# Performance work log

Hardware: AMD Instinct MI355X
Metric: run time of the kernel (lower is better)

The kernel has to match this reference:

```python
import jax, jax.numpy as jnp
import numpy as np

N_POINTS = 8192
N_TOPICS = 64
B = 524288


def setup_inputs() -> dict:
    key = jax.random.key(0)
    k1, k2, k3, k4 = jax.random.split(key, 4)
    pij = jax.random.uniform(k1, (B,), dtype=jnp.float32, minval=1e-6, maxval=1.0)
    i = jax.random.randint(k2, (B,), 0, N_POINTS, dtype=jnp.int64)
    j = jax.random.randint(k3, (B,), 0, N_POINTS, dtype=jnp.int64)
    W = jax.random.normal(k4, (N_POINTS, N_TOPICS), dtype=jnp.float32)  # nn.Embedding weight
    return {"pij": pij, "i": i, "j": j, "W": W}


def reference(pij, i, j, W):
    # pairwise squared distances over ALL points, via the gram trick
    # (avoids materializing the [n, n, d] broadcasted tensor of the torch code)
    sq = jnp.sum(W * W, axis=1)                       # [n]
    d2 = sq[:, None] + sq[None, :] - 2.0 * (W @ W.T)  # [n, n]
    d2 = jnp.maximum(d2, 0.0)                         # numerical floor (exact math is >= 0)
    n = W.shape[0]
    # Cauchy kernel partition: sum_{k,l} 1/(1+d2) minus the n diagonal ones
    part = jnp.sum(1.0 / (1.0 + d2)) - jnp.asarray(n, d2.dtype)
    xi = W[i]                                         # [B, d]
    xj = W[j]                                         # [B, d]
    # FAITHFUL to source: (1 + diff^2).sum(1) adds 1 per dim => n_topics + ||xi-xj||^2
    num = 1.0 / jnp.sum(1.0 + (xi - xj) ** 2, axis=1)  # [B]
    qij = num / part
    loss_kld = pij * (jnp.log(pij) - jnp.log(qij))
    return jnp.sum(loss_kld)
```

## Files before the change

kernel.cpp:

```cpp
#include <hip/hip_runtime.h>
#include <math.h>

#define NPOINTS   8192
#define NDIM      64
#define TILE      128
#define NT2       64
#define NBLK      2080
#define NGRP      512

#define WS_W16   0
#define WS_W8    262144
#define WS_SQ    393216
#define WS_PARTA 401408
#define WS_A1P   403488
#define WS_A3P   407584

typedef __attribute__((ext_vector_type(8))) short bf16x8;
typedef __attribute__((ext_vector_type(4))) float f32x4;
typedef __attribute__((ext_vector_type(2))) float f32x2;

__device__ inline unsigned f2bf_pk(float lo, float hi) {
    unsigned ul = __float_as_uint(lo), uh = __float_as_uint(hi);
    ul += 0x7FFFu + ((ul >> 16) & 1u);
    uh += 0x7FFFu + ((uh >> 16) & 1u);
    return (ul >> 16) | (uh & 0xFFFF0000u);
}
template <bool HI>
__device__ inline f32x2 cvt2(unsigned dw) {
    return __builtin_amdgcn_cvt_pk_f32_fp8((int)dw, HI);
}
__device__ inline void sqacc(f32x2& s, unsigned a, unsigned b) {
    f32x2 dl = cvt2<false>(a) - cvt2<false>(b);
    f32x2 dh = cvt2<true >(a) - cvt2<true >(b);
    s += dl * dl;
    s += dh * dh;
}

__global__ __launch_bounds__(256) void prep_kernel(const float* __restrict__ W,
                                                   float* __restrict__ sq,
                                                   unsigned* __restrict__ W16f,
                                                   unsigned* __restrict__ W8) {
    int g = blockIdx.x;
    int t = threadIdx.x;

    {
        int h = t >> 7, L = (t >> 1) & 63, dp = t & 1;
        int row = g * 16 + (L & 15), quad = L >> 4;
        float4 v = *(const float4*)(W + row * NDIM + h * 32 + quad * 8 + dp * 4);
        uint2 o;
        o.x = f2bf_pk(v.x, v.y);
        o.y = f2bf_pk(v.z, v.w);
        *(uint2*)(W16f + ((g * 2 + h) * 256 + L * 4 + dp * 2)) = o;
    }
    {
        int r = t >> 4, s = t & 15;
        float4 v = *(const float4*)(W + (g * 16 + r) * NDIM + s * 4);
        float p = v.x * v.x + v.y * v.y + v.z * v.z + v.w * v.w;
        p += __shfl_xor(p, 1, 64);
        p += __shfl_xor(p, 2, 64);
        p += __shfl_xor(p, 4, 64);
        p += __shfl_xor(p, 8, 64);
        if (s == 0) sq[g * 16 + r] = p;
    }
    {
        int r = g * 16 + (t >> 4), d = t & 15;
        float4 x = *(const float4*)(W + r * NDIM + d * 4);
        int lo = __builtin_amdgcn_cvt_pk_fp8_f32(x.x, x.y, 0, false);
        int dw = __builtin_amdgcn_cvt_pk_fp8_f32(x.z, x.w, lo, true);
        W8[r * 16 + d] = (unsigned)dw;
    }
}

__global__ __launch_bounds__(256) void pair_kernel(const unsigned* __restrict__ W8,
                                                   const float* __restrict__ pij,
                                                   const int* __restrict__ ii,
                                                   const int* __restrict__ jj,
                                                   int nb,
                                                   float* __restrict__ a1p,
                                                   float* __restrict__ a3p) {
    int t = threadIdx.x;
    int p = blockIdx.x * 256 + t;
    float a1 = 0.f, a3 = 0.f;
    if (p < nb) {
        int   i  = ii[p];
        int   j  = jj[p];
        float pv = pij[p];
        const uint4* X = (const uint4*)(W8 + i * 16);
        const uint4* Y = (const uint4*)(W8 + j * 16);
        uint4 x0 = X[0], x1 = X[1], x2 = X[2], x3 = X[3];
        uint4 y0 = Y[0], y1 = Y[1], y2 = Y[2], y3 = Y[3];
        f32x2 s2 = {0.f, 0.f};
        sqacc(s2, x0.x, y0.x); sqacc(s2, x0.y, y0.y);
        sqacc(s2, x0.z, y0.z); sqacc(s2, x0.w, y0.w);
        sqacc(s2, x1.x, y1.x); sqacc(s2, x1.y, y1.y);
        sqacc(s2, x1.z, y1.z); sqacc(s2, x1.w, y1.w);
        sqacc(s2, x2.x, y2.x); sqacc(s2, x2.y, y2.y);
        sqacc(s2, x2.z, y2.z); sqacc(s2, x2.w, y2.w);
        sqacc(s2, x3.x, y3.x); sqacc(s2, x3.y, y3.y);
        sqacc(s2, x3.z, y3.z); sqacc(s2, x3.w, y3.w);
        float v = s2.x + s2.y;
        a1 = pv * __logf(pv * ((float)NDIM + v));
        a3 = pv;
    }
    #pragma unroll
    for (int m = 32; m >= 1; m >>= 1) {
        a1 += __shfl_xor(a1, m, 64);
        a3 += __shfl_xor(a3, m, 64);
    }
    __shared__ float red[8];
    if ((t & 63) == 0) { red[t >> 6] = a1; red[4 + (t >> 6)] = a3; }
    __syncthreads();
    if (t == 0) {
        a1p[blockIdx.x] = red[0] + red[1] + red[2] + red[3];
        a3p[blockIdx.x] = red[4] + red[5] + red[6] + red[7];
    }
}

__global__ __launch_bounds__(256) void pairwise_kernel(const unsigned* __restrict__ W16f,
                                                       const float* __restrict__ sq,
                                                       float* __restrict__ partA) {
    int z = blockIdx.x;
    int t = threadIdx.x, w = t >> 6, lane = t & 63;
    int by = (int)((129.0f - sqrtf((float)(16641 - 8 * z))) * 0.5f);
    while (by * NT2 - by * (by - 1) / 2 > z) --by;
    while ((by + 1) * NT2 - (by + 1) * by / 2 <= z) ++by;
    int bx = by + (z - (by * NT2 - by * (by - 1) / 2));

    int wm = w >> 1, wn = w & 1, quad = lane >> 4, l15 = lane & 15;
    int a0 = by * TILE, b0 = bx * TILE;

    float4 base1[4];
    float  sqb[4];
    {
        int arow = a0 + wm * 64 + quad * 4;
        #pragma unroll
        for (int tm = 0; tm < 4; ++tm) {
            float4 v = *(const float4*)(sq + arow + tm * 16);
            base1[tm] = (float4){1.0f + v.x, 1.0f + v.y, 1.0f + v.z, 1.0f + v.w};
        }
        int bcol = b0 + wn * 64 + l15;
        #pragma unroll
        for (int tn = 0; tn < 4; ++tn) sqb[tn] = sq[bcol + tn * 16];
    }

    f32x4 acc[4][4];
    #pragma unroll
    for (int i = 0; i < 4; ++i)
        #pragma unroll
        for (int j = 0; j < 4; ++j) acc[i][j] = (f32x4){0.f, 0.f, 0.f, 0.f};

    int gA = (a0 >> 4) + wm * 4;
    int gB = (b0 >> 4) + wn * 4;
    #pragma unroll
    for (int h = 0; h < 2; ++h) {
        bf16x8 af[4], bfr[4];
        #pragma unroll
        for (int tm = 0; tm < 4; ++tm)
            af[tm] = *(const bf16x8*)(W16f + (((gA + tm) * 2 + h) * 256 + lane * 4));
        #pragma unroll
        for (int tn = 0; tn < 4; ++tn)
            bfr[tn] = *(const bf16x8*)(W16f + (((gB + tn) * 2 + h) * 256 + lane * 4));
        #pragma unroll
        for (int tm = 0; tm < 4; ++tm)
            #pragma unroll
            for (int tn = 0; tn < 4; ++tn)
                acc[tm][tn] = __builtin_amdgcn_mfma_f32_16x16x32_bf16(af[tm], bfr[tn],
                                                                      acc[tm][tn], 0, 0, 0);
    }

    float ssum = 0.f;
    if (bx > by) {
        #pragma unroll
        for (int tn = 0; tn < 4; ++tn) {
            float c0 = sqb[tn];
            #pragma unroll
            for (int tm = 0; tm < 4; ++tm) {
                ssum += __builtin_amdgcn_rcpf(fmaf(acc[tm][tn][0], -2.0f, base1[tm].x + c0));
                ssum += __builtin_amdgcn_rcpf(fmaf(acc[tm][tn][1], -2.0f, base1[tm].y + c0));
                ssum += __builtin_amdgcn_rcpf(fmaf(acc[tm][tn][2], -2.0f, base1[tm].z + c0));
                ssum += __builtin_amdgcn_rcpf(fmaf(acc[tm][tn][3], -2.0f, base1[tm].w + c0));
            }
        }
    } else {
        int quad4 = quad * 4;
        #pragma unroll
        for (int tn = 0; tn < 4; ++tn) {
            int cl = wn * 64 + tn * 16 + l15;
            float c0 = sqb[tn];
            float b4[4];
            #pragma unroll
            for (int tm = 0; tm < 4; ++tm) {
                b4[0] = base1[tm].x; b4[1] = base1[tm].y;
                b4[2] = base1[tm].z; b4[3] = base1[tm].w;
                #pragma unroll
                for (int r = 0; r < 4; ++r) {
                    int rl = wm * 64 + tm * 16 + quad4 + r;
                    float inv = __builtin_amdgcn_rcpf(fmaf(acc[tm][tn][r], -2.0f, b4[r] + c0));
                    ssum += (cl > rl) ? inv : 0.f;
                }
            }
        }
    }
    #pragma unroll
    for (int m = 32; m >= 1; m >>= 1) ssum += __shfl_xor(ssum, m, 64);
    __shared__ float wsum[4];
    if (lane == 0) wsum[w] = ssum;
    __syncthreads();
    if (t == 0) partA[z] = wsum[0] + wsum[1] + wsum[2] + wsum[3];
}

__global__ __launch_bounds__(256) void final_kernel(const float* __restrict__ partA,
                                                    const float* __restrict__ a1p,
                                                    const float* __restrict__ a3p,
                                                    int npb,
                                                    float* __restrict__ out) {
    __shared__ double r1[256], r2[256], r3[256];
    int t = threadIdx.x;
    double dpart = 0.0, d1 = 0.0, d3 = 0.0;
    for (int k = t; k < NBLK; k += 256) dpart += (double)partA[k];
    for (int k = t; k < npb; k += 256) { d1 += (double)a1p[k]; d3 += (double)a3p[k]; }
    r1[t] = dpart; r2[t] = d1; r3[t] = d3;
    __syncthreads();
    for (int s = 128; s >= 1; s >>= 1) {
        if (t < s) { r1[t] += r1[t + s]; r2[t] += r2[t + s]; r3[t] += r3[t + s]; }
        __syncthreads();
    }
    if (t == 0) {
        double part = 2.0 * r1[0];
        out[0] = (float)(r2[0] + r3[0] * log(part));
    }
}

extern "C" void kernel_launch(void* const* d_in, const int* in_sizes, int n_in,
                              void* d_out, int out_size, void* d_ws, size_t ws_size,
                              hipStream_t stream) {
    const float* pij = (const float*)d_in[0];
    const int*   ii  = (const int*)d_in[1];
    const int*   jj  = (const int*)d_in[2];
    const float* W   = (const float*)d_in[3];
    float* out = (float*)d_out;
    float* ws  = (float*)d_ws;

    unsigned* W16f  = (unsigned*)ws + WS_W16;
    unsigned* W8    = (unsigned*)ws + WS_W8;
    float*    sqv   = ws + WS_SQ;
    float*    partA = ws + WS_PARTA;
    float*    a1p   = ws + WS_A1P;
    float*    a3p   = ws + WS_A3P;

    int nb  = in_sizes[0];
    int npb = (nb + 255) / 256;

    prep_kernel<<<NGRP, 256, 0, stream>>>(W, sqv, W16f, W8);
    pair_kernel<<<npb, 256, 0, stream>>>(W8, pij, ii, jj, nb, a1p, a3p);
    pairwise_kernel<<<NBLK, 256, 0, stream>>>(W16f, sqv, partA);
    final_kernel<<<1, 256, 0, stream>>>(partA, a1p, a3p, npb, out);
}
```

Measured before the change: 90.65 us.

## Fuse pair, pairwise and final kernels into one launch with last-block reduction

```diff
diff --git a/kernel.cpp b/kernel.cpp
--- a/kernel.cpp
+++ b/kernel.cpp
@@ -14,6 +14,7 @@
 #define WS_PARTA 401408
 #define WS_A1P   403488
 #define WS_A3P   407584
+#define WS_CNT   411680
 
 typedef __attribute__((ext_vector_type(8))) short bf16x8;
 typedef __attribute__((ext_vector_type(4))) float f32x4;
@@ -35,13 +36,24 @@
     s += dl * dl;
     s += dh * dh;
 }
+__device__ inline float d2_16(const uint4 x[4], const uint4 y[4]) {
+    f32x2 s2 = {0.f, 0.f};
+    #pragma unroll
+    for (int k = 0; k < 4; ++k) {
+        sqacc(s2, x[k].x, y[k].x); sqacc(s2, x[k].y, y[k].y);
+        sqacc(s2, x[k].z, y[k].z); sqacc(s2, x[k].w, y[k].w);
+    }
+    return s2.x + s2.y;
+}
 
 __global__ __launch_bounds__(256) void prep_kernel(const float* __restrict__ W,
                                                    float* __restrict__ sq,
                                                    unsigned* __restrict__ W16f,
-                                                   unsigned* __restrict__ W8) {
+                                                   unsigned* __restrict__ W8,
+                                                   unsigned* __restrict__ cnt) {
     int g = blockIdx.x;
     int t = threadIdx.x;
+    if (g == 0 && t == 0) cnt[0] = 0u;
 
     {
         int h = t >> 7, L = (t >> 1) & 63, dp = t & 1;
@@ -71,154 +83,165 @@
     }
 }
 
-__global__ __launch_bounds__(256) void pair_kernel(const unsigned* __restrict__ W8,
-                                                   const float* __restrict__ pij,
-                                                   const int* __restrict__ ii,
-                                                   const int* __restrict__ jj,
-                                                   int nb,
-                                                   float* __restrict__ a1p,
-                                                   float* __restrict__ a3p) {
+__global__ __launch_bounds__(256) void fused_kernel(
+        const unsigned* __restrict__ W16f, const float* __restrict__ sq,
+        float* __restrict__ partA,
+        const unsigned* __restrict__ W8, const float* __restrict__ pij,
+        const int* __restrict__ ii, const int* __restrict__ jj, int nb,
+        float* __restrict__ a1p, float* __restrict__ a3p, int npb2,
+        unsigned* __restrict__ cnt, float* __restrict__ out) {
     int t = threadIdx.x;
-    int p = blockIdx.x * 256 + t;
-    float a1 = 0.f, a3 = 0.f;
-    if (p < nb) {
-        int   i  = ii[p];
-        int   j  = jj[p];
-        float pv = pij[p];
-        const uint4* X = (const uint4*)(W8 + i * 16);
-        const uint4* Y = (const uint4*)(W8 + j * 16);
-        uint4 x0 = X[0], x1 = X[1], x2 = X[2], x3 = X[3];
-        uint4 y0 = Y[0], y1 = Y[1], y2 = Y[2], y3 = Y[3];
-        f32x2 s2 = {0.f, 0.f};
-        sqacc(s2, x0.x, y0.x); sqacc(s2, x0.y, y0.y);
-        sqacc(s2, x0.z, y0.z); sqacc(s2, x0.w, y0.w);
-        sqacc(s2, x1.x, y1.x); sqacc(s2, x1.y, y1.y);
-        sqacc(s2, x1.z, y1.z); sqacc(s2, x1.w, y1.w);
-        sqacc(s2, x2.x, y2.x); sqacc(s2, x2.y, y2.y);
-        sqacc(s2, x2.z, y2.z); sqacc(s2, x2.w, y2.w);
-        sqacc(s2, x3.x, y3.x); sqacc(s2, x3.y, y3.y);
-        sqacc(s2, x3.z, y3.z); sqacc(s2, x3.w, y3.w);
-        float v = s2.x + s2.y;
-        a1 = pv * __logf(pv * ((float)NDIM + v));
-        a3 = pv;
-    }
-    #pragma unroll
-    for (int m = 32; m >= 1; m >>= 1) {
-        a1 += __shfl_xor(a1, m, 64);
-        a3 += __shfl_xor(a3, m, 64);
-    }
+    int z = blockIdx.x;
     __shared__ float red[8];
-    if ((t & 63) == 0) { red[t >> 6] = a1; red[4 + (t >> 6)] = a3; }
-    __syncthreads();
-    if (t == 0) {
-        a1p[blockIdx.x] = red[0] + red[1] + red[2] + red[3];
-        a3p[blockIdx.x] = red[4] + red[5] + red[6] + red[7];
-    }
-}
-
-__global__ __launch_bounds__(256) void pairwise_kernel(const unsigned* __restrict__ W16f,
-                                                       const float* __restrict__ sq,
-                                                       float* __restrict__ partA) {
-    int z = blockIdx.x;
-    int t = threadIdx.x, w = t >> 6, lane = t & 63;
-    int by = (int)((129.0f - sqrtf((float)(16641 - 8 * z))) * 0.5f);
-    while (by * NT2 - by * (by - 1) / 2 > z) --by;
-    while ((by + 1) * NT2 - (by + 1) * by / 2 <= z) ++by;
-    int bx = by + (z - (by * NT2 - by * (by - 1) / 2));
-
-    int wm = w >> 1, wn = w & 1, quad = lane >> 4, l15 = lane & 15;
-    int a0 = by * TILE, b0 = bx * TILE;
-
-    float4 base1[4];
-    float  sqb[4];
-    {
-        int arow = a0 + wm * 64 + quad * 4;
-        #pragma unroll
-        for (int tm = 0; tm < 4; ++tm) {
-            float4 v = *(const float4*)(sq + arow + tm * 16);
-            base1[tm] = (float4){1.0f + v.x, 1.0f + v.y, 1.0f + v.z, 1.0f + v.w};
-        }
-        int bcol = b0 + wn * 64 + l15;
-        #pragma unroll
-        for (int tn = 0; tn < 4; ++tn) sqb[tn] = sq[bcol + tn * 16];
-    }
-
-    f32x4 acc[4][4];
-    #pragma unroll
-    for (int i = 0; i < 4; ++i)
-        #pragma unroll
-        for (int j = 0; j < 4; ++j) acc[i][j] = (f32x4){0.f, 0.f, 0.f, 0.f};
-
-    int gA = (a0 >> 4) + wm * 4;
-    int gB = (b0 >> 4) + wn * 4;
-    #pragma unroll
-    for (int h = 0; h < 2; ++h) {
-        bf16x8 af[4], bfr[4];
-        #pragma unroll
-        for (int tm = 0; tm < 4; ++tm)
-            af[tm] = *(const bf16x8*)(W16f + (((gA + tm) * 2 + h) * 256 + lane * 4));
-        #pragma unroll
-        for (int tn = 0; tn < 4; ++tn)
-            bfr[tn] = *(const bf16x8*)(W16f + (((gB + tn) * 2 + h) * 256 + lane * 4));
-        #pragma unroll
-        for (int tm = 0; tm < 4; ++tm)
+    __shared__ float wsum[4];
+    __shared__ int lastFlag;
+
+    int twop = npb2 * 2;
+    bool isPair;
+    int job;
+    if (z < twop) { isPair = (z & 1) != 0; job = z >> 1; }
+    else          { isPair = false;        job = npb2 + (z - twop); }
+
+    if (isPair) {
+        int p1 = job * 512 + t;
+        int p2 = p1 + 256;
+        bool v1 = p1 < nb, v2 = p2 < nb;
+        int i1 = 0, j1 = 0, i2 = 0, j2 = 0;
+        float q1 = 0.f, q2 = 0.f;
+        if (v1) { i1 = ii[p1]; j1 = jj[p1]; q1 = pij[p1]; }
+        if (v2) { i2 = ii[p2]; j2 = jj[p2]; q2 = pij[p2]; }
+        const uint4* X1 = (const uint4*)(W8 + i1 * 16);
+        const uint4* Y1 = (const uint4*)(W8 + j1 * 16);
+        const uint4* X2 = (const uint4*)(W8 + i2 * 16);
+        const uint4* Y2 = (const uint4*)(W8 + j2 * 16);
+        uint4 xa[4], ya[4], xb[4], yb[4];
+        #pragma unroll
+        for (int k = 0; k < 4; ++k) xa[k] = X1[k];
+        #pragma unroll
+        for (int k = 0; k < 4; ++k) ya[k] = Y1[k];
+        #pragma unroll
+        for (int k = 0; k < 4; ++k) xb[k] = X2[k];
+        #pragma unroll
+        for (int k = 0; k < 4; ++k) yb[k] = Y2[k];
+        float a1 = 0.f, a3 = 0.f;
+        float da = d2_16(xa, ya);
+        float db = d2_16(xb, yb);
+        if (v1) { a1  = q1 * __logf(q1 * ((float)NDIM + da)); a3  = q1; }
+        if (v2) { a1 += q2 * __logf(q2 * ((float)NDIM + db)); a3 += q2; }
+        #pragma unroll
+        for (int m = 32; m >= 1; m >>= 1) {
+            a1 += __shfl_xor(a1, m, 64);
+            a3 += __shfl_xor(a3, m, 64);
+        }
+        if ((t & 63) == 0) { red[t >> 6] = a1; red[4 + (t >> 6)] = a3; }
+        __syncthreads();
+        if (t == 0) {
+            a1p[job] = red[0] + red[1] + red[2] + red[3];
+            a3p[job] = red[4] + red[5] + red[6] + red[7];
+        }
+    } else {
+        int zt = job;
+        int w = t >> 6, lane = t & 63;
+        int by = (int)((129.0f - sqrtf((float)(16641 - 8 * zt))) * 0.5f);
+        while (by * NT2 - by * (by - 1) / 2 > zt) --by;
+        while ((by + 1) * NT2 - (by + 1) * by / 2 <= zt) ++by;
+        int bx = by + (zt - (by * NT2 - by * (by - 1) / 2));
+
+        int wm = w >> 1, wn = w & 1, quad = lane >> 4, l15 = lane & 15;
+        int a0 = by * TILE, b0 = bx * TILE;
+
+        f32x4 acc[4][4];
+        #pragma unroll
+        for (int i = 0; i < 4; ++i)
+            #pragma unroll
+            for (int j = 0; j < 4; ++j) acc[i][j] = (f32x4){0.f, 0.f, 0.f, 0.f};
+
+        int gA = (a0 >> 4) + wm * 4;
+        int gB = (b0 >> 4) + wn * 4;
+        #pragma unroll
+        for (int h = 0; h < 2; ++h) {
+            bf16x8 af[4], bfr[4];
+            #pragma unroll
+            for (int tm = 0; tm < 4; ++tm)
+                af[tm] = *(const bf16x8*)(W16f + (((gA + tm) * 2 + h) * 256 + lane * 4));
             #pragma unroll
             for (int tn = 0; tn < 4; ++tn)
-                acc[tm][tn] = __builtin_amdgcn_mfma_f32_16x16x32_bf16(af[tm], bfr[tn],
-                                                                      acc[tm][tn], 0, 0, 0);
-    }
-
-    float ssum = 0.f;
-    if (bx > by) {
-        #pragma unroll
-        for (int tn = 0; tn < 4; ++tn) {
-            float c0 = sqb[tn];
+                bfr[tn] = *(const bf16x8*)(W16f + (((gB + tn) * 2 + h) * 256 + lane * 4));
+            #pragma unroll
+            for (int tm = 0; tm < 4; ++tm)
+                #pragma unroll
+                for (int tn = 0; tn < 4; ++tn)
+                    acc[tm][tn] = __builtin_amdgcn_mfma_f32_16x16x32_bf16(af[tm], bfr[tn],
+                                                                          acc[tm][tn], 0, 0, 0);
+        }
+
+        float4 base1[4];
+        float  sqb[4];
+        {
+            int arow = a0 + wm * 64 + quad * 4;
             #pragma unroll
             for (int tm = 0; tm < 4; ++tm) {
-                ssum += __builtin_amdgcn_rcpf(fmaf(acc[tm][tn][0], -2.0f, base1[tm].x + c0));
-                ssum += __builtin_amdgcn_rcpf(fmaf(acc[tm][tn][1], -2.0f, base1[tm].y + c0));
-                ssum += __builtin_amdgcn_rcpf(fmaf(acc[tm][tn][2], -2.0f, base1[tm].z + c0));
-                ssum += __builtin_amdgcn_rcpf(fmaf(acc[tm][tn][3], -2.0f, base1[tm].w + c0));
+                float4 v = *(const float4*)(sq + arow + tm * 16);
+                base1[tm] = (float4){1.0f + v.x, 1.0f + v.y, 1.0f + v.z, 1.0f + v.w};
             }
-        }
-    } else {
-        int quad4 = quad * 4;
-        #pragma unroll
-        for (int tn = 0; tn < 4; ++tn) {
-            int cl = wn * 64 + tn * 16 + l15;
-            float c0 = sqb[tn];
-            float b4[4];
-            #pragma unroll
-            for (int tm = 0; tm < 4; ++tm) {
-                b4[0] = base1[tm].x; b4[1] = base1[tm].y;
-                b4[2] = base1[tm].z; b4[3] = base1[tm].w;
+            int bcol = b0 + wn * 64 + l15;
+            #pragma unroll
+            for (int tn = 0; tn < 4; ++tn) sqb[tn] = sq[bcol + tn * 16];
+        }
+
+        float ssum = 0.f;
+        if (bx > by) {
+            #pragma unroll
+            for (int tn = 0; tn < 4; ++tn) {
+                float c0 = sqb[tn];
                 #pragma unroll
-                for (int r = 0; r < 4; ++r) {
-                    int rl = wm * 64 + tm * 16 + quad4 + r;
-                    float inv = __builtin_amdgcn_rcpf(fmaf(acc[tm][tn][r], -2.0f, b4[r] + c0));
-                    ssum += (cl > rl) ? inv : 0.f;
+                for (int tm = 0; tm < 4; ++tm) {
+                    ssum += __builtin_amdgcn_rcpf(fmaf(acc[tm][tn][0], -2.0f, base1[tm].x + c0));
+                    ssum += __builtin_amdgcn_rcpf(fmaf(acc[tm][tn][1], -2.0f, base1[tm].y + c0));
+                    ssum += __builtin_amdgcn_rcpf(fmaf(acc[tm][tn][2], -2.0f, base1[tm].z + c0));
+                    ssum += __builtin_amdgcn_rcpf(fmaf(acc[tm][tn][3], -2.0f, base1[tm].w + c0));
                 }
             }
-        }
-    }
-    #pragma unroll
-    for (int m = 32; m >= 1; m >>= 1) ssum += __shfl_xor(ssum, m, 64);
-    __shared__ float wsum[4];
-    if (lane == 0) wsum[w] = ssum;
+        } else {
+            int quad4 = quad * 4;
+            #pragma unroll
+            for (int tn = 0; tn < 4; ++tn) {
+                int cl = wn * 64 + tn * 16 + l15;
+                float c0 = sqb[tn];
+                float b4[4];
+                #pragma unroll
+                for (int tm = 0; tm < 4; ++tm) {
+                    b4[0] = base1[tm].x; b4[1] = base1[tm].y;
+                    b4[2] = base1[tm].z; b4[3] = base1[tm].w;
+                    #pragma unroll
+                    for (int r = 0; r < 4; ++r) {
+                        int rl = wm * 64 + tm * 16 + quad4 + r;
+                        float inv = __builtin_amdgcn_rcpf(fmaf(acc[tm][tn][r], -2.0f, b4[r] + c0));
+                        ssum += (cl > rl) ? inv : 0.f;
+                    }
+                }
+            }
+        }
+        #pragma unroll
+        for (int m = 32; m >= 1; m >>= 1) ssum += __shfl_xor(ssum, m, 64);
+        if (lane == 0) wsum[w] = ssum;
+        __syncthreads();
+        if (t == 0) partA[zt] = wsum[0] + wsum[1] + wsum[2] + wsum[3];
+    }
+
+    if (t == 0) {
+        __threadfence();
+        unsigned old = atomicAdd(cnt, 1u);
+        lastFlag = (old == (unsigned)(gridDim.x - 1)) ? 1 : 0;
+    }
     __syncthreads();
-    if (t == 0) partA[z] = wsum[0] + wsum[1] + wsum[2] + wsum[3];
-}
-
-__global__ __launch_bounds__(256) void final_kernel(const float* __restrict__ partA,
-                                                    const float* __restrict__ a1p,
-                                                    const float* __restrict__ a3p,
-                                                    int npb,
-                                                    float* __restrict__ out) {
+    if (!lastFlag) return;
+    __threadfence();
+
     __shared__ double r1[256], r2[256], r3[256];
-    int t = threadIdx.x;
     double dpart = 0.0, d1 = 0.0, d3 = 0.0;
     for (int k = t; k < NBLK; k += 256) dpart += (double)partA[k];
-    for (int k = t; k < npb; k += 256) { d1 += (double)a1p[k]; d3 += (double)a3p[k]; }
+    for (int k = t; k < npb2; k += 256) { d1 += (double)a1p[k]; d3 += (double)a3p[k]; }
     r1[t] = dpart; r2[t] = d1; r3[t] = d3;
     __syncthreads();
     for (int s = 128; s >= 1; s >>= 1) {
@@ -247,12 +270,13 @@
     float*    partA = ws + WS_PARTA;
     float*    a1p   = ws + WS_A1P;
     float*    a3p   = ws + WS_A3P;
-
-    int nb  = in_sizes[0];
-    int npb = (nb + 255) / 256;
-
-    prep_kernel<<<NGRP, 256, 0, stream>>>(W, sqv, W16f, W8);
-    pair_kernel<<<npb, 256, 0, stream>>>(W8, pij, ii, jj, nb, a1p, a3p);
-    pairwise_kernel<<<NBLK, 256, 0, stream>>>(W16f, sqv, partA);
-    final_kernel<<<1, 256, 0, stream>>>(partA, a1p, a3p, npb, out);
-}
+    unsigned* cnt   = (unsigned*)ws + WS_CNT;
+
+    int nb   = in_sizes[0];
+    int npb2 = (nb + 511) / 512;
+
+    prep_kernel<<<NGRP, 256, 0, stream>>>(W, sqv, W16f, W8, cnt);
+    fused_kernel<<<NBLK + npb2, 256, 0, stream>>>(W16f, sqv, partA,
+                                                  W8, pij, ii, jj, nb,
+                                                  a1p, a3p, npb2, cnt, out);
+}
```

Measured after the change: 157.4 us. 73.6% more time.
